# Kernel optimization log

Hardware: AMD Instinct MI355X
Metric: run time of the kernel (lower is better)

The kernel has to match this reference:

```python
import jax, jax.numpy as jnp
import numpy as np

HIDDEN = 1024
D_INNER = 2048
DT_RANK = 64
STATE = 16
KCONV = 4


def setup_inputs() -> dict:
    key = jax.random.key(0)
    ks = jax.random.split(key, 9)
    s = lambda k, shape, sc=0.02: jax.random.normal(k, shape, dtype=jnp.float32) * sc
    return {
        "x": jax.random.normal(ks[0], (2, 1024, HIDDEN), dtype=jnp.float32),
        "in_proj_w": s(ks[1], (2 * D_INNER, HIDDEN)),
        "conv_w": s(ks[2], (D_INNER, 1, KCONV), 0.2),
        "conv_b": s(ks[3], (D_INNER,), 0.1),
        "x_proj_w": s(ks[4], (DT_RANK + 2 * STATE, D_INNER)),
        "dt_proj_w": s(ks[5], (D_INNER, DT_RANK), 0.1),
        "dt_proj_b": s(ks[6], (D_INNER,), 0.1),
        "A_log": s(ks[7], (D_INNER, STATE), 0.5),
        "out_proj_w": s(ks[8], (HIDDEN, D_INNER)),
    }


def _selective_scan(u, delta, A, B, C):
    # u, delta: (b,l,d); A: (d,n); B, C: (b,l,n)
    deltaA = jnp.exp(delta[..., None] * A)               # (b,l,d,n)
    dBu = (delta * u)[..., None] * B[:, :, None, :]      # (b,l,d,n)
    # scan over time axis; carry h: (b,d,n)
    deltaA_t = jnp.moveaxis(deltaA, 1, 0)                # (l,b,d,n)
    dBu_t = jnp.moveaxis(dBu, 1, 0)                      # (l,b,d,n)
    C_t = jnp.moveaxis(C, 1, 0)                          # (l,b,n)

    def step(h, inp):
        dA_i, dBu_i, C_i = inp
        h = dA_i * h + dBu_i
        y = jnp.einsum('bdn,bn->bd', h, C_i)
        return h, y

    h0 = jnp.zeros(u.shape[:1] + u.shape[2:] + (A.shape[1],), dtype=u.dtype)
    _, ys = jax.lax.scan(step, h0, (deltaA_t, dBu_t, C_t))
    return jnp.moveaxis(ys, 0, 1)                        # (b,l,d)


def reference(x, in_proj_w, conv_w, conv_b, x_proj_w, dt_proj_w, dt_proj_b, A_log, out_proj_w):
    b, l, _ = x.shape
    xr = x @ in_proj_w.T                                 # (b,l,2*d_inner)
    xs, res = jnp.split(xr, 2, axis=-1)
    # causal depthwise conv1d: pad left k-1 (matches padding=k-1 then [:l])
    xc = jnp.moveaxis(xs, 1, 2)                          # (b,d,l)
    xc = jax.lax.conv_general_dilated(
        xc, conv_w, window_strides=(1,), padding=[(KCONV - 1, 0)],
        feature_group_count=D_INNER,
        dimension_numbers=('NCH', 'OIH', 'NCH'))
    xc = xc + conv_b[None, :, None]
    xs = jnp.moveaxis(xc, 2, 1)                          # (b,l,d)
    xs = jax.nn.silu(xs)
    x_dbl = xs @ x_proj_w.T                              # (b,l,dt_rank+2n)
    dt, B, C = jnp.split(x_dbl, [DT_RANK, DT_RANK + STATE], axis=-1)
    delta = jax.nn.softplus(dt @ dt_proj_w.T + dt_proj_b)
    A = -jnp.exp(A_log.astype(jnp.float32))
    y = _selective_scan(xs, delta, A, B, C)
    y = y * jax.nn.silu(res)
    return y @ out_proj_w.T
```

## Files before the change

### kernel.cpp

```cpp
#include <hip/hip_runtime.h>

typedef unsigned short u16;
typedef __bf16 bf16x8 __attribute__((ext_vector_type(8)));
typedef float f32x4 __attribute__((ext_vector_type(4)));

__device__ inline float bf2f(u16 u) {
    unsigned int x = ((unsigned int)u) << 16;
    return __builtin_bit_cast(float, x);
}
__device__ inline u16 f2bf(float f) {
    unsigned int x = __builtin_bit_cast(unsigned int, f);
    return (u16)((x + 0x7FFFu + ((x >> 16) & 1u)) >> 16);
}
__device__ inline float sigm(float v) { return 1.f / (1.f + __expf(-v)); }

__device__ inline uint4 pack8(const float* p) {
    const float4* q = (const float4*)p;
    float4 a = q[0], b = q[1];
    union { u16 h[8]; uint4 v; } u;
    u.h[0] = f2bf(a.x); u.h[1] = f2bf(a.y); u.h[2] = f2bf(a.z); u.h[3] = f2bf(a.w);
    u.h[4] = f2bf(b.x); u.h[5] = f2bf(b.y); u.h[6] = f2bf(b.z); u.h[7] = f2bf(b.w);
    return u.v;
}

__global__ __launch_bounds__(256)
void cvt_bf16(const float* __restrict__ in, u16* __restrict__ out)
{
    int i = blockIdx.x * 256 + threadIdx.x;
    ((uint4*)out)[i] = pack8(in + (size_t)i * 8);
}
__global__ __launch_bounds__(256)
void cvt_pad_xproj(const float* __restrict__ in, u16* __restrict__ out)
{
    int i = blockIdx.x * 256 + threadIdx.x;
    int row = (i * 8) >> 11;
    ((uint4*)out)[i] = (row < 96) ? pack8(in + (size_t)row * 2048 + ((i * 8) & 2047))
                                  : make_uint4(0u, 0u, 0u, 0u);
}

template<int EPI, bool OUTF32>
__global__ __launch_bounds__(256, 2)
void gemm2(const u16* __restrict__ A, int lda,
           const u16* __restrict__ B, int ldb,
           void* __restrict__ Cout, int ldc,
           int N, int ksplit, size_t zElems,
           const float* __restrict__ bias)
{
    __shared__ u16 sA[128][40];
    __shared__ u16 sB[128][40];

    const int tid  = threadIdx.x;
    const int lane = tid & 63;
    const int wave = tid >> 6;
    const int wm = (wave >> 1) * 64;
    const int wn = (wave & 1) * 64;
    const int m0 = blockIdx.y * 128;
    const int n0 = blockIdx.x * 128;
    const int lm = lane & 15;
    const int kq = (lane >> 4) * 8;
    const int k0 = blockIdx.z * ksplit;

    const int r0 = tid >> 2, q0 = (tid & 3) * 8;
    const int r1 = (tid + 256) >> 2, q1 = ((tid + 256) & 3) * 8;
    const u16* gA0 = A + (size_t)(m0 + r0) * lda + k0 + q0;
    const u16* gA1 = A + (size_t)(m0 + r1) * lda + k0 + q1;
    const u16* gB0 = B + (size_t)(n0 + r0) * ldb + k0 + q0;
    const u16* gB1 = B + (size_t)(n0 + r1) * ldb + k0 + q1;

    f32x4 acc[4][4] = {};

    uint4 pa0 = *(const uint4*)gA0, pa1 = *(const uint4*)gA1;
    uint4 pb0 = *(const uint4*)gB0, pb1 = *(const uint4*)gB1;

    for (int kb = 0; kb < ksplit; kb += 32) {
        *(uint4*)&sA[r0][q0] = pa0;
        *(uint4*)&sA[r1][q1] = pa1;
        *(uint4*)&sB[r0][q0] = pb0;
        *(uint4*)&sB[r1][q1] = pb1;
        __syncthreads();

        if (kb + 32 < ksplit) {
            pa0 = *(const uint4*)(gA0 + kb + 32);
            pa1 = *(const uint4*)(gA1 + kb + 32);
            pb0 = *(const uint4*)(gB0 + kb + 32);
            pb1 = *(const uint4*)(gB1 + kb + 32);
        }

        bf16x8 af[4], bfr[4];
        #pragma unroll
        for (int i = 0; i < 4; ++i)
            af[i] = *(const bf16x8*)&sA[wm + i * 16 + lm][kq];
        #pragma unroll
        for (int j = 0; j < 4; ++j)
            bfr[j] = *(const bf16x8*)&sB[wn + j * 16 + lm][kq];
        #pragma unroll
        for (int i = 0; i < 4; ++i)
            #pragma unroll
            for (int j = 0; j < 4; ++j)
                acc[i][j] = __builtin_amdgcn_mfma_f32_16x16x32_bf16(af[i], bfr[j], acc[i][j], 0, 0, 0);
        __syncthreads();
    }

    #pragma unroll
    for (int i = 0; i < 4; ++i) {
        int crow = m0 + wm + i * 16 + ((lane >> 4) << 2);
        #pragma unroll
        for (int j = 0; j < 4; ++j) {
            int ccol = n0 + wn + j * 16 + lm;
            if (ccol < N) {
                #pragma unroll
                for (int r = 0; r < 4; ++r) {
                    float v = acc[i][j][r];
                    if (EPI == 1) { v += bias[ccol]; v = (v > 20.f) ? v : log1pf(__expf(v)); }
                    if (EPI == 2 && ccol >= 2048) v *= sigm(v);
                    size_t off = (size_t)blockIdx.z * zElems + (size_t)(crow + r) * ldc + ccol;
                    if (OUTF32) ((float*)Cout)[off] = v;
                    else        ((u16*)Cout)[off]   = f2bf(v);
                }
            }
        }
    }
}

__global__ __launch_bounds__(256)
void reduce96(const float* __restrict__ splits, u16* __restrict__ xdbl)
{
    int i = blockIdx.x * 256 + threadIdx.x;
    float acc = 0.f;
    #pragma unroll
    for (int z = 0; z < 8; ++z) acc += splits[(size_t)z * 196608 + i];
    xdbl[i] = f2bf(acc);
}

__global__ __launch_bounds__(256)
void reduce_out(const u16* __restrict__ parts, float* __restrict__ out)
{
    int i = blockIdx.x * 256 + threadIdx.x;
    float acc[8] = {};
    #pragma unroll
    for (int z = 0; z < 4; ++z) {
        uint4 v = ((const uint4*)(parts + (size_t)z * 2097152))[i];
        const u16* h = (const u16*)&v;
        #pragma unroll
        for (int e = 0; e < 8; ++e) acc[e] += bf2f(h[e]);
    }
    float4* o = (float4*)(out + (size_t)i * 8);
    o[0] = make_float4(acc[0], acc[1], acc[2], acc[3]);
    o[1] = make_float4(acc[4], acc[5], acc[6], acc[7]);
}

__global__ __launch_bounds__(256)
void conv_silu(const u16* __restrict__ xr, const float* __restrict__ w,
               const float* __restrict__ bias, u16* __restrict__ xs)
{
    int idx = blockIdx.x * 256 + threadIdx.x;
    int d = idx & 2047, t = (idx >> 11) & 1023, b = idx >> 21;
    const u16* base = xr + (size_t)b * 1024 * 4096;
    float acc = bias[d];
    #pragma unroll
    for (int j = 0; j < 4; ++j) {
        int ti = t - 3 + j;
        if (ti >= 0) acc = fmaf(w[d * 4 + j], bf2f(base[(size_t)ti * 4096 + d]), acc);
    }
    xs[idx] = f2bf(acc * sigm(acc));
}

template<int PHC>
__global__ __launch_bounds__(256)
void scan_chunk(const u16* __restrict__ deltag, u16* __restrict__ xsg,
                const u16* __restrict__ xdbl, const float* __restrict__ A_log,
                const u16* __restrict__ xr, float* __restrict__ summ,
                float* __restrict__ ssum)
{
    const int tid = threadIdx.x;
    const int d0 = blockIdx.x * 256;
    const int c  = blockIdx.y;
    const int b  = blockIdx.z;
    const int d  = d0 + tid;
    const int tok0 = b * 1024 + c * 32;

    __shared__ u16 s_del[32][256];
    __shared__ u16 s_uu[32][256];
    __shared__ u16 s_bc[32][32];
    __shared__ u16 s_res[PHC ? 32 : 1][PHC ? 256 : 1];
    __shared__ u16 s_y[PHC ? 32 : 1][PHC ? 256 : 1];

    for (int i = tid; i < 1024; i += 256) {
        int tl = i >> 5, v = i & 31;
        size_t tok = (size_t)(tok0 + tl);
        *(uint4*)&s_del[tl][v * 8] = *(const uint4*)&deltag[tok * 4096 + d0 + v * 8];
        *(uint4*)&s_uu[tl][v * 8]  = *(const uint4*)&xsg[tok * 2048 + d0 + v * 8];
        if (PHC)
            *(uint4*)&s_res[tl][v * 8] = *(const uint4*)&xr[tok * 4096 + 2048 + d0 + v * 8];
    }
    for (int i = tid; i < 1024; i += 256) {
        int tl = i >> 5, j = i & 31;
        s_bc[tl][j] = xdbl[(size_t)(tok0 + tl) * 96 + 64 + j];
    }

    float Ar[16], h[16];
    {
        const float4* Ap = (const float4*)(A_log + (size_t)d * 16);
        #pragma unroll
        for (int q = 0; q < 4; ++q) {
            float4 a = Ap[q];
            Ar[q * 4 + 0] = -__expf(a.x); Ar[q * 4 + 1] = -__expf(a.y);
            Ar[q * 4 + 2] = -__expf(a.z); Ar[q * 4 + 3] = -__expf(a.w);
        }
    }
    if (PHC) {
        const float4* hp = (const float4*)&summ[((size_t)(b * 32 + c) * 2048 + d) * 16];
        #pragma unroll
        for (int q = 0; q < 4; ++q) {
            float4 v = hp[q];
            h[q * 4 + 0] = v.x; h[q * 4 + 1] = v.y; h[q * 4 + 2] = v.z; h[q * 4 + 3] = v.w;
        }
    } else {
        #pragma unroll
        for (int n = 0; n < 16; ++n) h[n] = 0.f;
    }
    __syncthreads();

    float S = 0.f;
    #pragma unroll 4
    for (int tl = 0; tl < 32; ++tl) {
        float dlt = bf2f(s_del[tl][tid]);
        float du = dlt * bf2f(s_uu[tl][tid]);
        if (!PHC) S += dlt;
        #pragma unroll
        for (int n = 0; n < 16; ++n)
            h[n] = fmaf(__expf(dlt * Ar[n]), h[n], du * bf2f(s_bc[tl][n]));
        if (PHC) {
            float y = 0.f;
            #pragma unroll
            for (int n = 0; n < 16; ++n)
                y = fmaf(h[n], bf2f(s_bc[tl][16 + n]), y);
            s_y[tl][tid] = f2bf(y * bf2f(s_res[tl][tid]));
        }
    }

    if (!PHC) {
        float4* bp = (float4*)&summ[((size_t)(b * 32 + c) * 2048 + d) * 16];
        #pragma unroll
        for (int q = 0; q < 4; ++q)
            bp[q] = make_float4(h[q * 4], h[q * 4 + 1], h[q * 4 + 2], h[q * 4 + 3]);
        ssum[(size_t)(b * 32 + c) * 2048 + d] = S;
    } else {
        __syncthreads();
        for (int i = tid; i < 1024; i += 256) {
            int tl = i >> 5, v = i & 31;
            *(uint4*)&xsg[(size_t)(tok0 + tl) * 2048 + d0 + v * 8] = *(uint4*)&s_y[tl][v * 8];
        }
    }
}

__global__ __launch_bounds__(256)
void scan_phaseB(float* __restrict__ summ, const float* __restrict__ ssum,
                 const float* __restrict__ A_log)
{
    int g = blockIdx.x * 256 + threadIdx.x;
    int n = g & 15;
    int d = (g >> 4) & 2047;
    int b = g >> 15;
    float An = -__expf(A_log[(size_t)d * 16 + n]);
    float h = 0.f;
    for (int c = 0; c < 32; ++c) {
        size_t idx = ((size_t)(b * 32 + c) * 2048 + d) * 16 + n;
        float bc = summ[idx];
        float Sc = ssum[(size_t)(b * 32 + c) * 2048 + d];
        summ[idx] = h;
        h = fmaf(__expf(An * Sc), h, bc);
    }
}

__global__ void sentinel_kernel(float* out, float v) { out[0] = v; }

extern "C" void kernel_launch(void* const* d_in, const int* in_sizes, int n_in,
                              void* d_out, int out_size, void* d_ws, size_t ws_size,
                              hipStream_t stream)
{
    const float* x         = (const float*)d_in[0];
    const float* in_w      = (const float*)d_in[1];
    const float* conv_w    = (const float*)d_in[2];
    const float* conv_b    = (const float*)d_in[3];
    const float* xproj_w   = (const float*)d_in[4];
    const float* dtproj_w  = (const float*)d_in[5];
    const float* dtproj_b  = (const float*)d_in[6];
    const float* A_log     = (const float*)d_in[7];
    const float* outproj_w = (const float*)d_in[8];
    float* out = (float*)d_out;

    static const int EXP[9] = {2097152, 4194304, 8192, 2048, 196608, 131072, 2048, 32768, 2097152};
    int bad = -1;
    if (n_in != 9) bad = 9;
    else { for (int i = 0; i < 9; ++i) if (in_sizes[i] != EXP[i]) { bad = i; break; } }
    if (bad < 0 && out_size != 2097152) bad = 10;
    if (bad < 0 && ws_size < 34734080u) bad = 11;
    if (bad >= 0) {
        sentinel_kernel<<<1, 1, 0, stream>>>(out, 131072.f * (1.f + (float)bad / 16.f));
        return;
    }

    char* ws = (char*)d_ws;
    u16*   xr      = (u16*)(ws);
    u16*   xs      = (u16*)(ws + 16777216);
    u16*   xdbl    = (u16*)(ws + 25165824);
    char*  R       = ws + 25559040;
    u16*   x_bf    = xs;
    u16*   inw_bf  = (u16*)(R);
    u16*   xpw_bf  = (u16*)(R + 8388608);
    u16*   dtw_bf  = (u16*)(R + 8912896);
    float* splits  = (float*)(R);
    float* summ    = (float*)(R);
    float* ssum    = (float*)(R + 8388608);
    u16*   opw_bf  = (u16*)(R);
    u16*   oparts  = xr;

    cvt_bf16<<<1024, 256, 0, stream>>>(x, x_bf);
    cvt_bf16<<<2048, 256, 0, stream>>>(in_w, inw_bf);
    cvt_pad_xproj<<<128, 256, 0, stream>>>(xproj_w, xpw_bf);
    cvt_bf16<<<64, 256, 0, stream>>>(dtproj_w, dtw_bf);
    gemm2<2, false><<<dim3(32, 16, 1), 256, 0, stream>>>(
        x_bf, 1024, inw_bf, 1024, xr, 4096, 4096, 1024, 0, nullptr);
    conv_silu<<<16384, 256, 0, stream>>>(xr, conv_w, conv_b, xs);
    gemm2<0, true><<<dim3(1, 16, 8), 256, 0, stream>>>(
        xs, 2048, xpw_bf, 2048, splits, 96, 96, 256, 196608, nullptr);
    reduce96<<<768, 256, 0, stream>>>(splits, xdbl);
    gemm2<1, false><<<dim3(16, 16, 1), 256, 0, stream>>>(
        xdbl, 96, dtw_bf, 64, xr, 4096, 2048, 64, 0, dtproj_b);
    scan_chunk<0><<<dim3(8, 32, 2), 256, 0, stream>>>(xr, xs, xdbl, A_log, xr, summ, ssum);
    scan_phaseB<<<256, 256, 0, stream>>>(summ, ssum, A_log);
    scan_chunk<1><<<dim3(8, 32, 2), 256, 0, stream>>>(xr, xs, xdbl, A_log, xr, summ, ssum);
    cvt_bf16<<<1024, 256, 0, stream>>>(outproj_w, opw_bf);
    gemm2<0, false><<<dim3(8, 16, 4), 256, 0, stream>>>(
        xs, 2048, opw_bf, 2048, oparts, 1024, 1024, 512, 2097152, nullptr);
    reduce_out<<<1024, 256, 0, stream>>>(oparts, out);
}
```

Before: 262.6 us.

## Fuse weight conversions into one kernel and deepen GEMM K-tile to 64

Merges the five fp32-to-bf16 conversion launches into a single kernel, giving each buffer its own region in a larger workspace. The GEMM now stages a K-tile of 64 instead of 32, which halves the number of barrier pairs per K step and doubles the MFMA work done per LDS fill. The x_proj GEMM split-K goes from 8 to 16 slices with a matching 16-way reduce. In exchange it uses more LDS per block and registers for the wider prefetch, and needs a larger workspace.

New measurement: 338.0 us. +28.7%, slower.

```diff
diff --git a/kernel.cpp b/kernel.cpp
--- a/kernel.cpp
+++ b/kernel.cpp
@@ -24,30 +24,44 @@
 }
 
 __global__ __launch_bounds__(256)
-void cvt_bf16(const float* __restrict__ in, u16* __restrict__ out)
+void cvt_all(const float* __restrict__ x, const float* __restrict__ in_w,
+             const float* __restrict__ xproj_w, const float* __restrict__ dtw,
+             const float* __restrict__ opw,
+             u16* __restrict__ x_bf, u16* __restrict__ inw_bf,
+             u16* __restrict__ xpw_bf, u16* __restrict__ dtw_bf,
+             u16* __restrict__ opw_bf)
 {
     int i = blockIdx.x * 256 + threadIdx.x;
-    ((uint4*)out)[i] = pack8(in + (size_t)i * 8);
-}
-__global__ __launch_bounds__(256)
-void cvt_pad_xproj(const float* __restrict__ in, u16* __restrict__ out)
-{
-    int i = blockIdx.x * 256 + threadIdx.x;
-    int row = (i * 8) >> 11;
-    ((uint4*)out)[i] = (row < 96) ? pack8(in + (size_t)row * 2048 + ((i * 8) & 2047))
-                                  : make_uint4(0u, 0u, 0u, 0u);
+    if (i < 262144) {
+        ((uint4*)x_bf)[i] = pack8(x + (size_t)i * 8);
+    } else if (i < 786432) {
+        int j = i - 262144;
+        ((uint4*)inw_bf)[j] = pack8(in_w + (size_t)j * 8);
+    } else if (i < 819200) {
+        int j = i - 786432;
+        int row = j >> 8;
+        ((uint4*)xpw_bf)[j] = (row < 96)
+            ? pack8(xproj_w + (size_t)row * 2048 + (j & 255) * 8)
+            : make_uint4(0u, 0u, 0u, 0u);
+    } else if (i < 835584) {
+        int j = i - 819200;
+        ((uint4*)dtw_bf)[j] = pack8(dtw + (size_t)j * 8);
+    } else {
+        int j = i - 835584;
+        ((uint4*)opw_bf)[j] = pack8(opw + (size_t)j * 8);
+    }
 }
 
 template<int EPI, bool OUTF32>
 __global__ __launch_bounds__(256, 2)
-void gemm2(const u16* __restrict__ A, int lda,
-           const u16* __restrict__ B, int ldb,
-           void* __restrict__ Cout, int ldc,
-           int N, int ksplit, size_t zElems,
-           const float* __restrict__ bias)
-{
-    __shared__ u16 sA[128][40];
-    __shared__ u16 sB[128][40];
+void gemm64(const u16* __restrict__ A, int lda,
+            const u16* __restrict__ B, int ldb,
+            void* __restrict__ Cout, int ldc,
+            int N, int ksplit, size_t zElems,
+            const float* __restrict__ bias)
+{
+    __shared__ u16 sA[128][72];
+    __shared__ u16 sB[128][72];
 
     const int tid  = threadIdx.x;
     const int lane = tid & 63;
@@ -60,44 +74,54 @@
     const int kq = (lane >> 4) * 8;
     const int k0 = blockIdx.z * ksplit;
 
-    const int r0 = tid >> 2, q0 = (tid & 3) * 8;
-    const int r1 = (tid + 256) >> 2, q1 = ((tid + 256) & 3) * 8;
-    const u16* gA0 = A + (size_t)(m0 + r0) * lda + k0 + q0;
-    const u16* gA1 = A + (size_t)(m0 + r1) * lda + k0 + q1;
-    const u16* gB0 = B + (size_t)(n0 + r0) * ldb + k0 + q0;
-    const u16* gB1 = B + (size_t)(n0 + r1) * ldb + k0 + q1;
+    int row[4], qc[4];
+    const u16 *ga[4], *gb[4];
+    #pragma unroll
+    for (int s = 0; s < 4; ++s) {
+        int c = tid + s * 256;
+        row[s] = c >> 3;
+        qc[s] = (c & 7) * 8;
+        ga[s] = A + (size_t)(m0 + row[s]) * lda + k0 + qc[s];
+        gb[s] = B + (size_t)(n0 + row[s]) * ldb + k0 + qc[s];
+    }
 
     f32x4 acc[4][4] = {};
 
-    uint4 pa0 = *(const uint4*)gA0, pa1 = *(const uint4*)gA1;
-    uint4 pb0 = *(const uint4*)gB0, pb1 = *(const uint4*)gB1;
-
-    for (int kb = 0; kb < ksplit; kb += 32) {
-        *(uint4*)&sA[r0][q0] = pa0;
-        *(uint4*)&sA[r1][q1] = pa1;
-        *(uint4*)&sB[r0][q0] = pb0;
-        *(uint4*)&sB[r1][q1] = pb1;
+    uint4 pa[4], pb[4];
+    #pragma unroll
+    for (int s = 0; s < 4; ++s) { pa[s] = *(const uint4*)ga[s]; pb[s] = *(const uint4*)gb[s]; }
+
+    for (int kb = 0; kb < ksplit; kb += 64) {
+        #pragma unroll
+        for (int s = 0; s < 4; ++s) {
+            *(uint4*)&sA[row[s]][qc[s]] = pa[s];
+            *(uint4*)&sB[row[s]][qc[s]] = pb[s];
+        }
         __syncthreads();
 
-        if (kb + 32 < ksplit) {
-            pa0 = *(const uint4*)(gA0 + kb + 32);
-            pa1 = *(const uint4*)(gA1 + kb + 32);
-            pb0 = *(const uint4*)(gB0 + kb + 32);
-            pb1 = *(const uint4*)(gB1 + kb + 32);
-        }
-
-        bf16x8 af[4], bfr[4];
-        #pragma unroll
-        for (int i = 0; i < 4; ++i)
-            af[i] = *(const bf16x8*)&sA[wm + i * 16 + lm][kq];
-        #pragma unroll
-        for (int j = 0; j < 4; ++j)
-            bfr[j] = *(const bf16x8*)&sB[wn + j * 16 + lm][kq];
-        #pragma unroll
-        for (int i = 0; i < 4; ++i)
+        if (kb + 64 < ksplit) {
+            #pragma unroll
+            for (int s = 0; s < 4; ++s) {
+                pa[s] = *(const uint4*)(ga[s] + kb + 64);
+                pb[s] = *(const uint4*)(gb[s] + kb + 64);
+            }
+        }
+
+        #pragma unroll
+        for (int ks = 0; ks < 2; ++ks) {
+            bf16x8 af[4], bfr[4];
+            #pragma unroll
+            for (int i = 0; i < 4; ++i)
+                af[i] = *(const bf16x8*)&sA[wm + i * 16 + lm][ks * 32 + kq];
             #pragma unroll
             for (int j = 0; j < 4; ++j)
-                acc[i][j] = __builtin_amdgcn_mfma_f32_16x16x32_bf16(af[i], bfr[j], acc[i][j], 0, 0, 0);
+                bfr[j] = *(const bf16x8*)&sB[wn + j * 16 + lm][ks * 32 + kq];
+            #pragma unroll
+            for (int i = 0; i < 4; ++i)
+                #pragma unroll
+                for (int j = 0; j < 4; ++j)
+                    acc[i][j] = __builtin_amdgcn_mfma_f32_16x16x32_bf16(af[i], bfr[j], acc[i][j], 0, 0, 0);
+        }
         __syncthreads();
     }
 
@@ -128,7 +152,7 @@
     int i = blockIdx.x * 256 + threadIdx.x;
     float acc = 0.f;
     #pragma unroll
-    for (int z = 0; z < 8; ++z) acc += splits[(size_t)z * 196608 + i];
+    for (int z = 0; z < 16; ++z) acc += splits[(size_t)z * 196608 + i];
     xdbl[i] = f2bf(acc);
 }
 
@@ -295,44 +319,40 @@
     if (n_in != 9) bad = 9;
     else { for (int i = 0; i < 9; ++i) if (in_sizes[i] != EXP[i]) { bad = i; break; } }
     if (bad < 0 && out_size != 2097152) bad = 10;
-    if (bad < 0 && ws_size < 34734080u) bad = 11;
+    if (bad < 0 && ws_size < 64618496u) bad = 11;
     if (bad >= 0) {
         sentinel_kernel<<<1, 1, 0, stream>>>(out, 131072.f * (1.f + (float)bad / 16.f));
         return;
     }
 
     char* ws = (char*)d_ws;
-    u16*   xr      = (u16*)(ws);
-    u16*   xs      = (u16*)(ws + 16777216);
-    u16*   xdbl    = (u16*)(ws + 25165824);
-    char*  R       = ws + 25559040;
-    u16*   x_bf    = xs;
-    u16*   inw_bf  = (u16*)(R);
-    u16*   xpw_bf  = (u16*)(R + 8388608);
-    u16*   dtw_bf  = (u16*)(R + 8912896);
-    float* splits  = (float*)(R);
-    float* summ    = (float*)(R);
-    float* ssum    = (float*)(R + 8388608);
-    u16*   opw_bf  = (u16*)(R);
-    u16*   oparts  = xr;
-
-    cvt_bf16<<<1024, 256, 0, stream>>>(x, x_bf);
-    cvt_bf16<<<2048, 256, 0, stream>>>(in_w, inw_bf);
-    cvt_pad_xproj<<<128, 256, 0, stream>>>(xproj_w, xpw_bf);
-    cvt_bf16<<<64, 256, 0, stream>>>(dtproj_w, dtw_bf);
-    gemm2<2, false><<<dim3(32, 16, 1), 256, 0, stream>>>(
+    u16*   xr     = (u16*)(ws);
+    u16*   xs     = (u16*)(ws + 16777216);
+    u16*   xdbl   = (u16*)(ws + 25165824);
+    u16*   x_bf   = (u16*)(ws + 25559040);
+    u16*   inw_bf = (u16*)(ws + 29753344);
+    u16*   xpw_bf = (u16*)(ws + 38141952);
+    u16*   dtw_bf = (u16*)(ws + 38666240);
+    u16*   opw_bf = (u16*)(ws + 38928384);
+    float* splits = (float*)(ws + 43122688);
+    float* summ   = (float*)(ws + 55705600);
+    float* ssum   = (float*)(ws + 64094208);
+    u16*   oparts = xr;
+
+    cvt_all<<<4288, 256, 0, stream>>>(x, in_w, xproj_w, dtproj_w, outproj_w,
+                                      x_bf, inw_bf, xpw_bf, dtw_bf, opw_bf);
+    gemm64<2, false><<<dim3(32, 16, 1), 256, 0, stream>>>(
         x_bf, 1024, inw_bf, 1024, xr, 4096, 4096, 1024, 0, nullptr);
     conv_silu<<<16384, 256, 0, stream>>>(xr, conv_w, conv_b, xs);
-    gemm2<0, true><<<dim3(1, 16, 8), 256, 0, stream>>>(
-        xs, 2048, xpw_bf, 2048, splits, 96, 96, 256, 196608, nullptr);
+    gemm64<0, true><<<dim3(1, 16, 16), 256, 0, stream>>>(
+        xs, 2048, xpw_bf, 2048, splits, 96, 96, 128, 196608, nullptr);
     reduce96<<<768, 256, 0, stream>>>(splits, xdbl);
-    gemm2<1, false><<<dim3(16, 16, 1), 256, 0, stream>>>(
+    gemm64<1, false><<<dim3(16, 16, 1), 256, 0, stream>>>(
         xdbl, 96, dtw_bf, 64, xr, 4096, 2048, 64, 0, dtproj_b);
     scan_chunk<0><<<dim3(8, 32, 2), 256, 0, stream>>>(xr, xs, xdbl, A_log, xr, summ, ssum);
     scan_phaseB<<<256, 256, 0, stream>>>(summ, ssum, A_log);
     scan_chunk<1><<<dim3(8, 32, 2), 256, 0, stream>>>(xr, xs, xdbl, A_log, xr, summ, ssum);
-    cvt_bf16<<<1024, 256, 0, stream>>>(outproj_w, opw_bf);
-    gemm2<0, false><<<dim3(8, 16, 4), 256, 0, stream>>>(
+    gemm64<0, false><<<dim3(8, 16, 4), 256, 0, stream>>>(
         xs, 2048, opw_bf, 2048, oparts, 1024, 1024, 512, 2097152, nullptr);
     reduce_out<<<1024, 256, 0, stream>>>(oparts, out);
 }
```
